# Kernel optimization log

Measured on AMD Instinct MI355X. Metric: run time of the kernel, lower is better.

Reference implementation:

```python
import math
import jax, jax.numpy as jnp
import numpy as np

G = 96       # grid side; N = G*G tokens, one token per grid cell
D = 512      # d_model
R = 2        # radius (Chebyshev)
LN_EPS = 1e-5

# 24 neighbor offsets in the (2R+1)^2 window, excluding (0,0) (self is excluded in the torch code)
_OFF = np.array([(dx, dy) for dx in range(-R, R + 1) for dy in range(-R, R + 1) if not (dx == 0 and dy == 0)], dtype=np.int32)


def _layer_norm(x, g, b):
    m = jnp.mean(x, axis=-1, keepdims=True)
    v = jnp.mean(jnp.square(x - m), axis=-1, keepdims=True)
    return (x - m) * jax.lax.rsqrt(v + LN_EPS) * g + b


def setup_inputs() -> dict:
    key = jax.random.key(0)
    ks = jax.random.split(key, 12)
    N = G * G
    x = jax.random.normal(ks[0], (N, D), jnp.float32)
    gx, gy = jnp.meshgrid(jnp.arange(G), jnp.arange(G), indexing='ij')
    grid = jnp.stack([gx.ravel(), gy.ravel()], axis=-1).astype(jnp.int32)  # [N,2], one token per cell

    def lin(k, din, dout):
        return jax.random.normal(k, (din, dout), jnp.float32) * (1.0 / math.sqrt(din))

    return {
        'x': x, 'grid': grid,
        'Wq': lin(ks[1], D, D), 'bq': jnp.zeros((D,), jnp.float32),
        'Wk': lin(ks[2], D, D), 'bk': jnp.zeros((D,), jnp.float32),
        'Wv': lin(ks[3], D, D), 'bv': jnp.zeros((D,), jnp.float32),
        'Wo': lin(ks[4], D, D), 'bo': jnp.zeros((D,), jnp.float32),
        'g1': jnp.ones((D,), jnp.float32), 'b1': jnp.zeros((D,), jnp.float32),
        'g2': jnp.ones((D,), jnp.float32), 'b2': jnp.zeros((D,), jnp.float32),
        'W1': lin(ks[5], D, 4 * D), 'bf1': jnp.zeros((4 * D,), jnp.float32),
        'W2': lin(ks[6], 4 * D, D), 'bf2': jnp.zeros((D,), jnp.float32),
    }


def reference(x, grid, Wq, bq, Wk, bk, Wv, bv, Wo, bo, g1, b1, g2, b2, W1, bf1, W2, bf2):
    # dropout is identity (eval mode)
    h = _layer_norm(x, g1, b1)
    q = h @ Wq + bq
    k = h @ Wk + bk
    v = h @ Wv + bv

    off = jnp.asarray(_OFF)                      # [K=24, 2]
    nx = grid[:, 0:1] + off[None, :, 0]          # [N, K]
    ny = grid[:, 1:2] + off[None, :, 1]
    valid = (nx >= 0) & (nx < G) & (ny >= 0) & (ny < G)
    idx = jnp.where(valid, nx * G + ny, 0)       # row-major cell -> token index

    k_nbr = k[idx]                               # [N, K, D]
    v_nbr = v[idx]                               # [N, K, D]
    scores = jnp.einsum('nd,nkd->nk', q, k_nbr) / math.sqrt(D)
    neg = jnp.finfo(scores.dtype).min
    scores = jnp.where(valid, scores, neg)
    attn = jax.nn.softmax(scores, axis=-1)       # every token has >=8 valid neighbors for G>R
    out = jnp.einsum('nk,nkd->nd', attn, v_nbr)  # [N, D]

    x = x + out @ Wo + bo
    h2 = _layer_norm(x, g2, b2)
    ffn = jax.nn.gelu(h2 @ W1 + bf1, approximate=False) @ W2 + bf2
    return x + ffn
```

## Files before the change

### kernel.cpp

```cpp
#include <hip/hip_runtime.h>

typedef unsigned short u16;
typedef unsigned int u32;
typedef __bf16 bf16x8 __attribute__((ext_vector_type(8)));
typedef float f32x4 __attribute__((ext_vector_type(4)));

#define GRID_G 96
#define DMODEL 512
#define NTOK (GRID_G * GRID_G)

__device__ __forceinline__ u16 f2bf(float f) {
  return __builtin_bit_cast(u16, (__bf16)f);
}
__device__ __forceinline__ void unpack8(uint4 u, float* f) {
  f[0] = __builtin_bit_cast(float, u.x << 16);
  f[1] = __builtin_bit_cast(float, u.x & 0xffff0000u);
  f[2] = __builtin_bit_cast(float, u.y << 16);
  f[3] = __builtin_bit_cast(float, u.y & 0xffff0000u);
  f[4] = __builtin_bit_cast(float, u.z << 16);
  f[5] = __builtin_bit_cast(float, u.z & 0xffff0000u);
  f[6] = __builtin_bit_cast(float, u.w << 16);
  f[7] = __builtin_bit_cast(float, u.w & 0xffff0000u);
}
__device__ __forceinline__ float gelu_fast(float x) {
  float y = 0.7978845608f * (x + 0.044715f * x * x * x);
  float a = fabsf(y);
  float e = __expf(-2.0f * a);
  float th = (1.0f - e) / (1.0f + e);
  th = __builtin_copysignf(th, y);
  return 0.5f * x * (1.0f + th);
}

__device__ __forceinline__ void tr_tile(const float* __restrict__ src,
                                        u16* __restrict__ dst, int R, int C,
                                        int bx, int by, float (*tile)[33]) {
  int tx = threadIdx.x & 31, ty = threadIdx.x >> 5;
#pragma unroll
  for (int i = 0; i < 4; ++i) {
    int r = ty + i * 8;
    tile[r][tx] = src[(size_t)(by * 32 + r) * C + (bx * 32 + tx)];
  }
  __syncthreads();
#pragma unroll
  for (int i = 0; i < 4; ++i) {
    int c = ty + i * 8;
    dst[(size_t)(bx * 32 + c) * R + (by * 32 + tx)] = f2bf(tile[tx][c]);
  }
}

__global__ __launch_bounds__(256) void k_prep(
    const float* __restrict__ Wq, const float* __restrict__ Wk,
    const float* __restrict__ Wv, const float* __restrict__ Wo,
    const float* __restrict__ W1, const float* __restrict__ W2,
    const float* __restrict__ bq, const float* __restrict__ bk,
    const float* __restrict__ bv, const float* __restrict__ x,
    const float* __restrict__ g1, const float* __restrict__ b1,
    u16* __restrict__ WQT, u16* __restrict__ WKT, u16* __restrict__ WVT,
    u16* __restrict__ WOT, u16* __restrict__ W1T, u16* __restrict__ W2T,
    float* __restrict__ BCAT, u16* __restrict__ H) {
  __shared__ float tile[32][33];
  const int b = blockIdx.x;
  if (b < 1024) {
    int z = b >> 8, sub = b & 255;
    const float* s = z == 0 ? Wq : z == 1 ? Wk : z == 2 ? Wv : Wo;
    u16* d = z == 0 ? WQT : z == 1 ? WKT : z == 2 ? WVT : WOT;
    tr_tile(s, d, 512, 512, sub & 15, sub >> 4, tile);
  } else if (b < 2048) {
    int idx = b - 1024;
    tr_tile(W1, W1T, 512, 2048, idx & 63, idx >> 6, tile);
  } else if (b < 3072) {
    int idx = b - 2048;
    tr_tile(W2, W2T, 2048, 512, idx & 15, idx >> 4, tile);
  } else if (b < 3078) {
    int i = (b - 3072) * 256 + threadIdx.x;
    if (i < 512) BCAT[i] = bq[i];
    else if (i < 1024) BCAT[i] = bk[i - 512];
    else if (i < 1536) BCAT[i] = bv[i - 1024];
  } else {
    int tid = threadIdx.x, wid = tid >> 6, lane = tid & 63;
    int row = (b - 3078) * 4 + wid;
    const float* xr = x + (size_t)row * DMODEL;
    float4 v0 = *(const float4*)(xr + lane * 4);
    float4 v1 = *(const float4*)(xr + 256 + lane * 4);
    float s = v0.x + v0.y + v0.z + v0.w + v1.x + v1.y + v1.z + v1.w;
    float sq = v0.x * v0.x + v0.y * v0.y + v0.z * v0.z + v0.w * v0.w +
               v1.x * v1.x + v1.y * v1.y + v1.z * v1.z + v1.w * v1.w;
#pragma unroll
    for (int m = 1; m < 64; m <<= 1) {
      s += __shfl_xor(s, m);
      sq += __shfl_xor(sq, m);
    }
    float mean = s * (1.0f / DMODEL);
    float rstd = rsqrtf(sq * (1.0f / DMODEL) - mean * mean + 1e-5f);
    float4 ga = *(const float4*)(g1 + lane * 4);
    float4 gb = *(const float4*)(g1 + 256 + lane * 4);
    float4 ba = *(const float4*)(b1 + lane * 4);
    float4 bb = *(const float4*)(b1 + 256 + lane * 4);
    ushort4 o0, o1;
    o0.x = f2bf((v0.x - mean) * rstd * ga.x + ba.x);
    o0.y = f2bf((v0.y - mean) * rstd * ga.y + ba.y);
    o0.z = f2bf((v0.z - mean) * rstd * ga.z + ba.z);
    o0.w = f2bf((v0.w - mean) * rstd * ga.w + ba.w);
    o1.x = f2bf((v1.x - mean) * rstd * gb.x + bb.x);
    o1.y = f2bf((v1.y - mean) * rstd * gb.y + bb.y);
    o1.z = f2bf((v1.z - mean) * rstd * gb.z + bb.z);
    o1.w = f2bf((v1.w - mean) * rstd * gb.w + bb.w);
    u16* op = H + (size_t)row * DMODEL;
    *(ushort4*)(op + lane * 4) = o0;
    *(ushort4*)(op + 256 + lane * 4) = o1;
  }
}

__global__ __launch_bounds__(256) void k_layernorm_bf16(
    const float* __restrict__ x, const float* __restrict__ g,
    const float* __restrict__ b, u16* __restrict__ out) {
  int tid = threadIdx.x, wid = tid >> 6, lane = tid & 63;
  int row = blockIdx.x * 4 + wid;
  const float* xr = x + (size_t)row * DMODEL;
  float4 v0 = *(const float4*)(xr + lane * 4);
  float4 v1 = *(const float4*)(xr + 256 + lane * 4);
  float s = v0.x + v0.y + v0.z + v0.w + v1.x + v1.y + v1.z + v1.w;
  float sq = v0.x * v0.x + v0.y * v0.y + v0.z * v0.z + v0.w * v0.w +
             v1.x * v1.x + v1.y * v1.y + v1.z * v1.z + v1.w * v1.w;
#pragma unroll
  for (int m = 1; m < 64; m <<= 1) {
    s += __shfl_xor(s, m);
    sq += __shfl_xor(sq, m);
  }
  float mean = s * (1.0f / DMODEL);
  float rstd = rsqrtf(sq * (1.0f / DMODEL) - mean * mean + 1e-5f);
  float4 ga = *(const float4*)(g + lane * 4);
  float4 gb = *(const float4*)(g + 256 + lane * 4);
  float4 ba = *(const float4*)(b + lane * 4);
  float4 bb = *(const float4*)(b + 256 + lane * 4);
  ushort4 o0, o1;
  o0.x = f2bf((v0.x - mean) * rstd * ga.x + ba.x);
  o0.y = f2bf((v0.y - mean) * rstd * ga.y + ba.y);
  o0.z = f2bf((v0.z - mean) * rstd * ga.z + ba.z);
  o0.w = f2bf((v0.w - mean) * rstd * ga.w + ba.w);
  o1.x = f2bf((v1.x - mean) * rstd * gb.x + bb.x);
  o1.y = f2bf((v1.y - mean) * rstd * gb.y + bb.y);
  o1.z = f2bf((v1.z - mean) * rstd * gb.z + bb.z);
  o1.w = f2bf((v1.w - mean) * rstd * gb.w + bb.w);
  u16* op = out + (size_t)row * DMODEL;
  *(ushort4*)(op + lane * 4) = o0;
  *(ushort4*)(op + 256 + lane * 4) = o1;
}

__global__ __launch_bounds__(256) void k_attn(
    const u16* __restrict__ q, const u16* __restrict__ kk,
    const u16* __restrict__ vv, const int* __restrict__ gpos,
    u16* __restrict__ out) {
  int tid = threadIdx.x, wid = tid >> 6, lane = tid & 63;
  int n = blockIdx.x * 4 + wid;
  int px = gpos[2 * n], py = gpos[2 * n + 1];
  float qf[8];
  unpack8(*(const uint4*)(q + (size_t)n * DMODEL + lane * 8), qf);
  float sc[24];
  int nid[24];
  bool ok[24];
#pragma unroll
  for (int j = 0; j < 24; ++j) {
    int jj = j < 12 ? j : j + 1;
    int dx = jj / 5 - 2, dy = jj % 5 - 2;
    int nx = px + dx, ny = py + dy;
    bool val = (nx >= 0) && (nx < GRID_G) && (ny >= 0) && (ny < GRID_G);
    int id = val ? nx * GRID_G + ny : 0;
    ok[j] = val;
    nid[j] = id;
    float kf[8];
    unpack8(*(const uint4*)(kk + (size_t)id * DMODEL + lane * 8), kf);
    float p = 0.f;
#pragma unroll
    for (int e = 0; e < 8; ++e) p += qf[e] * kf[e];
#pragma unroll
    for (int m = 1; m < 64; m <<= 1) p += __shfl_xor(p, m);
    sc[j] = p * 0.04419417382415922f;
  }
  float mx = -3.0e38f;
#pragma unroll
  for (int j = 0; j < 24; ++j)
    if (ok[j]) mx = fmaxf(mx, sc[j]);
  float wsum = 0.f, w[24];
#pragma unroll
  for (int j = 0; j < 24; ++j) {
    w[j] = ok[j] ? expf(sc[j] - mx) : 0.f;
    wsum += w[j];
  }
  float inv = 1.0f / wsum;
  float acc[8] = {0, 0, 0, 0, 0, 0, 0, 0};
#pragma unroll
  for (int j = 0; j < 24; ++j) {
    float vf[8];
    unpack8(*(const uint4*)(vv + (size_t)nid[j] * DMODEL + lane * 8), vf);
    float wj = w[j];
#pragma unroll
    for (int e = 0; e < 8; ++e) acc[e] += wj * vf[e];
  }
  uint4 o;
  o.x = (u32)f2bf(acc[0] * inv) | ((u32)f2bf(acc[1] * inv) << 16);
  o.y = (u32)f2bf(acc[2] * inv) | ((u32)f2bf(acc[3] * inv) << 16);
  o.z = (u32)f2bf(acc[4] * inv) | ((u32)f2bf(acc[5] * inv) << 16);
  o.w = (u32)f2bf(acc[6] * inv) | ((u32)f2bf(acc[7] * inv) << 16);
  *(uint4*)(out + (size_t)n * DMODEL + lane * 8) = o;
}

#define BARR { __builtin_amdgcn_s_barrier(); __builtin_amdgcn_sched_barrier(0); }
#define WAIT8 asm volatile("s_waitcnt vmcnt(8)" ::: "memory");
#define WAIT0 asm volatile("s_waitcnt vmcnt(0)" ::: "memory");
#define LGKM0 asm volatile("s_waitcnt lgkmcnt(0)" ::: "memory");

template <int EPI>
__global__ __launch_bounds__(256, 2) void k_gemm(
    const u16* __restrict__ A, const u16* __restrict__ Bt,
    const float* __restrict__ bias, const float* __restrict__ res,
    float* __restrict__ outF, u16* __restrict__ outB,
    int M, int N, int K, int tiles_n) {
  __shared__ u16 lds[32768];
  const int t = threadIdx.x, wid = t >> 6, lane = t & 63;
  const int nwg = gridDim.x, bid = blockIdx.x;
  const int l = ((bid & 7) * (nwg >> 3)) + (bid >> 3);
  const int bM = (l / tiles_n) * 128, bN = (l % tiles_n) * 128;
  const int wr = wid >> 1, wc = wid & 1, lr = lane & 15, lg = lane >> 4;

  const int rs = lane >> 3;
  const int cl = (lane & 7) ^ rs;
  const u16* gA[4];
  const u16* gB[4];
  int dstL[4];
#pragma unroll
  for (int j = 0; j < 4; ++j) {
    int r = wid * 32 + j * 8 + rs;
    gA[j] = A + (size_t)(bM + r) * K + cl * 8;
    gB[j] = Bt + (size_t)(bN + r) * K + cl * 8;
    dstL[j] = wid * 2048 + j * 512;
  }

#define STAGE1(BUF, KOFF)                                                             \
  {                                                                                   \
    _Pragma("unroll") for (int j = 0; j < 4; ++j) {                                   \
      __builtin_amdgcn_global_load_lds(                                               \
          (const __attribute__((address_space(1))) void*)(gA[j] + (KOFF)),            \
          (__attribute__((address_space(3))) void*)(lds + (BUF)*16384 + dstL[j]),     \
          16, 0, 0);                                                                  \
      __builtin_amdgcn_global_load_lds(                                               \
          (const __attribute__((address_space(1))) void*)(gB[j] + (KOFF)),            \
          (__attribute__((address_space(3))) void*)(lds + (BUF)*16384 + 8192 + dstL[j]), \
          16, 0, 0);                                                                  \
    }                                                                                 \
  }

  const int offA0 = (wr * 64 + lr) * 64 + ((0 + lg) ^ (lr & 7)) * 8;
  const int offA1 = (wr * 64 + lr) * 64 + ((4 + lg) ^ (lr & 7)) * 8;
  const int offB0 = (wc * 64 + lr) * 64 + ((0 + lg) ^ (lr & 7)) * 8;
  const int offB1 = (wc * 64 + lr) * 64 + ((4 + lg) ^ (lr & 7)) * 8;

  f32x4 acc[4][4];
#pragma unroll
  for (int i = 0; i < 4; ++i)
#pragma unroll
    for (int j = 0; j < 4; ++j) acc[i][j] = (f32x4){0.f, 0.f, 0.f, 0.f};

#define COMPUTE1(BUF)                                                                 \
  {                                                                                   \
    _Pragma("unroll") for (int ks = 0; ks < 2; ++ks) {                                \
      const int oa = (BUF)*16384 + (ks ? offA1 : offA0);                              \
      const int ob = (BUF)*16384 + 8192 + (ks ? offB1 : offB0);                       \
      bf16x8 af[4], bfr[4];                                                           \
      _Pragma("unroll") for (int mt = 0; mt < 4; ++mt)                                \
          af[mt] = __builtin_bit_cast(bf16x8, *(const uint4*)(lds + oa + mt * 1024)); \
      _Pragma("unroll") for (int nt = 0; nt < 4; ++nt)                                \
          bfr[nt] = __builtin_bit_cast(bf16x8, *(const uint4*)(lds + ob + nt * 1024));\
      _Pragma("unroll") for (int mt = 0; mt < 4; ++mt)                                \
          _Pragma("unroll") for (int nt = 0; nt < 4; ++nt)                            \
              acc[mt][nt] = __builtin_amdgcn_mfma_f32_16x16x32_bf16(                  \
                  af[mt], bfr[nt], acc[mt][nt], 0, 0, 0);                             \
    }                                                                                 \
  }

  const int nk = K >> 6;
  STAGE1(0, 0);
  int koff = 64;
  for (int tt = 0; tt < nk; tt += 2) {
    if (tt + 1 < nk) { STAGE1(1, koff); WAIT8 } else { WAIT0 }
    BARR;
    COMPUTE1(0);
    BARR;
    if (tt + 2 < nk) { STAGE1(0, koff + 64); WAIT8 } else { WAIT0 }
    BARR;
    COMPUTE1(1);
    BARR;
    koff += 128;
  }
#undef STAGE1
#undef COMPUTE1

#pragma unroll
  for (int mt = 0; mt < 4; ++mt) {
#pragma unroll
    for (int nt = 0; nt < 4; ++nt) {
      int col = bN + wc * 64 + nt * 16 + lr;
      float bc = bias[col];
      int row0 = bM + wr * 64 + mt * 16 + lg * 4;
#pragma unroll
      for (int r = 0; r < 4; ++r) {
        float val = acc[mt][nt][r] + bc;
        size_t off = (size_t)(row0 + r) * N + col;
        if constexpr (EPI == 1) {
          outF[off] = res[off] + val;
        } else {
          outB[off] = f2bf(val);
        }
      }
    }
  }
}

template <int EPI>
__global__ __launch_bounds__(256, 4) void k_gemm_hi(
    const u16* __restrict__ A, const u16* __restrict__ Bt,
    const float* __restrict__ bias, u16* __restrict__ outB,
    int M, int N, int K, int tiles_n) {
  __shared__ u16 lds[16384];
  const int t = threadIdx.x, wid = t >> 6, lane = t & 63;
  const int nwg = gridDim.x, bid = blockIdx.x;
  const int l = ((bid & 7) * (nwg >> 3)) + (bid >> 3);
  const int bM = (l / tiles_n) * 128, bN = (l % tiles_n) * 128;
  const int wr = wid >> 1, wc = wid & 1, lr = lane & 15, lg = lane >> 4;

  const int rs = lane >> 3;
  const int cl = (lane & 7) ^ rs;
  const u16* gA[4];
  const u16* gB[4];
  int dstL[4];
#pragma unroll
  for (int j = 0; j < 4; ++j) {
    int r = wid * 32 + j * 8 + rs;
    gA[j] = A + (size_t)(bM + r) * K + cl * 8;
    gB[j] = Bt + (size_t)(bN + r) * K + cl * 8;
    dstL[j] = wid * 2048 + j * 512;
  }

  const int offA0 = (wr * 64 + lr) * 64 + ((0 + lg) ^ (lr & 7)) * 8;
  const int offA1 = (wr * 64 + lr) * 64 + ((4 + lg) ^ (lr & 7)) * 8;
  const int offB0 = 8192 + (wc * 64 + lr) * 64 + ((0 + lg) ^ (lr & 7)) * 8;
  const int offB1 = 8192 + (wc * 64 + lr) * 64 + ((4 + lg) ^ (lr & 7)) * 8;

  f32x4 acc[4][4];
#pragma unroll
  for (int i = 0; i < 4; ++i)
#pragma unroll
    for (int j = 0; j < 4; ++j) acc[i][j] = (f32x4){0.f, 0.f, 0.f, 0.f};

  const int nk = K >> 6;
  for (int tt = 0; tt < nk; ++tt) {
    const int koff = tt << 6;
#pragma unroll
    for (int j = 0; j < 4; ++j) {
      __builtin_amdgcn_global_load_lds(
          (const __attribute__((address_space(1))) void*)(gA[j] + koff),
          (__attribute__((address_space(3))) void*)(lds + dstL[j]), 16, 0, 0);
      __builtin_amdgcn_global_load_lds(
          (const __attribute__((address_space(1))) void*)(gB[j] + koff),
          (__attribute__((address_space(3))) void*)(lds + 8192 + dstL[j]), 16, 0, 0);
    }
    WAIT0;
    BARR;
#pragma unroll
    for (int ks = 0; ks < 2; ++ks) {
      const int oa = ks ? offA1 : offA0;
      const int ob = ks ? offB1 : offB0;
      bf16x8 af[4], bfr[4];
#pragma unroll
      for (int mt = 0; mt < 4; ++mt)
        af[mt] = __builtin_bit_cast(bf16x8, *(const uint4*)(lds + oa + mt * 1024));
#pragma unroll
      for (int nt = 0; nt < 4; ++nt)
        bfr[nt] = __builtin_bit_cast(bf16x8, *(const uint4*)(lds + ob + nt * 1024));
#pragma unroll
      for (int mt = 0; mt < 4; ++mt)
#pragma unroll
        for (int nt = 0; nt < 4; ++nt)
          acc[mt][nt] = __builtin_amdgcn_mfma_f32_16x16x32_bf16(af[mt], bfr[nt], acc[mt][nt], 0, 0, 0);
    }
    LGKM0;
    BARR;
  }

#pragma unroll
  for (int mt = 0; mt < 4; ++mt) {
#pragma unroll
    for (int nt = 0; nt < 4; ++nt) {
      int col = bN + wc * 64 + nt * 16 + lr;
      float bc = bias[col];
      int row0 = bM + wr * 64 + mt * 16 + lg * 4;
#pragma unroll
      for (int r = 0; r < 4; ++r) {
        float val = acc[mt][nt][r] + bc;
        if constexpr (EPI == 2) {
          outB[(size_t)(row0 + r) * N + col] = f2bf(gelu_fast(val));
        } else {
          int seg = col >> 9;
          size_t off = (size_t)seg * ((size_t)NTOK * DMODEL) +
                       (size_t)(row0 + r) * DMODEL + (col & 511);
          outB[off] = f2bf(val);
        }
      }
    }
  }
}

extern "C" void kernel_launch(void* const* d_in, const int* in_sizes, int n_in,
                              void* d_out, int out_size, void* d_ws, size_t ws_size,
                              hipStream_t stream) {
  const float* x = (const float*)d_in[0];
  const int* gpos = (const int*)d_in[1];
  const float* Wq = (const float*)d_in[2];
  const float* bq = (const float*)d_in[3];
  const float* Wk = (const float*)d_in[4];
  const float* bk = (const float*)d_in[5];
  const float* Wv = (const float*)d_in[6];
  const float* bv = (const float*)d_in[7];
  const float* Wo = (const float*)d_in[8];
  const float* bo = (const float*)d_in[9];
  const float* g1 = (const float*)d_in[10];
  const float* b1 = (const float*)d_in[11];
  const float* g2 = (const float*)d_in[12];
  const float* b2 = (const float*)d_in[13];
  const float* W1 = (const float*)d_in[14];
  const float* bf1 = (const float*)d_in[15];
  const float* W2 = (const float*)d_in[16];
  const float* bf2 = (const float*)d_in[17];
  float* out = (float*)d_out;
  char* ws = (char*)d_ws;

  constexpr size_t SZ_W512 = (size_t)512 * 512 * 2;
  constexpr size_t SZ_W2048 = (size_t)512 * 2048 * 2;
  constexpr size_t SZ_ACT = (size_t)NTOK * 512 * 2;

  u16* WQT = (u16*)(ws + 0);
  u16* WKT = (u16*)(ws + SZ_W512);
  u16* WVT = (u16*)(ws + 2 * SZ_W512);
  u16* WOT = (u16*)(ws + 3 * SZ_W512);
  u16* W1T = (u16*)(ws + 4 * SZ_W512);
  u16* W2T = (u16*)(ws + 4 * SZ_W512 + SZ_W2048);
  float* BCAT = (float*)(ws + 4 * SZ_W512 + 2 * SZ_W2048);
  char* actbase = ws + 4 * SZ_W512 + 2 * SZ_W2048 + 6144;
  u16* H = (u16*)(actbase);
  u16* Q = (u16*)(actbase + SZ_ACT);
  u16* KB = (u16*)(actbase + 2 * SZ_ACT);
  u16* VB = (u16*)(actbase + 3 * SZ_ACT);
  u16* H2 = (u16*)(actbase + 4 * SZ_ACT);
  u16* U = (u16*)(actbase);

  k_prep<<<5382, 256, 0, stream>>>(Wq, Wk, Wv, Wo, W1, W2, bq, bk, bv, x, g1, b1,
                                   WQT, WKT, WVT, WOT, W1T, W2T, BCAT, H);

  k_gemm_hi<3><<<864, 256, 0, stream>>>(H, WQT, BCAT, Q, NTOK, 1536, 512, 12);

  k_attn<<<NTOK / 4, 256, 0, stream>>>(Q, KB, VB, gpos, H);

  k_gemm<1><<<288, 256, 0, stream>>>(H, WOT, bo, x, out, nullptr, NTOK, 512, 512, 4);

  k_layernorm_bf16<<<NTOK / 4, 256, 0, stream>>>(out, g2, b2, H2);

  k_gemm_hi<2><<<1152, 256, 0, stream>>>(H2, W1T, bf1, U, NTOK, 2048, 512, 16);

  k_gemm<1><<<288, 256, 0, stream>>>(U, W2T, bf2, out, out, nullptr, NTOK, 512, 2048, 4);
}
```

Baseline: 158.9 us.

## Use 256x128 GEMM tiles with 8 waves sharing B tile, fast softmax intrinsics

The QKV and FFN1 GEMMs move from 128x128 tiles with 4 waves to 256x128 tiles with 8 waves. The B tile is loaded into LDS once and shared across twice as many rows, which cuts global and L2 traffic for the weights and halves the grid size. K is now a template constant so the loop bound is known at compile time. The attention softmax also switches to the fast __expf and a hardware reciprocal, trading a little accuracy for fewer instructions; the larger LDS footprint and 512-thread blocks may lower occupancy.

After: 156.1 us. No clear change (-1.7%).

```diff
diff --git a/kernel.cpp b/kernel.cpp
--- a/kernel.cpp
+++ b/kernel.cpp
@@ -184,10 +184,10 @@
   float wsum = 0.f, w[24];
 #pragma unroll
   for (int j = 0; j < 24; ++j) {
-    w[j] = ok[j] ? expf(sc[j] - mx) : 0.f;
+    w[j] = ok[j] ? __expf(sc[j] - mx) : 0.f;
     wsum += w[j];
   }
-  float inv = 1.0f / wsum;
+  float inv = __builtin_amdgcn_rcpf(wsum);
   float acc[8] = {0, 0, 0, 0, 0, 0, 0, 0};
 #pragma unroll
   for (int j = 0; j < 24; ++j) {
@@ -316,35 +316,28 @@
   }
 }
 
-template <int EPI>
-__global__ __launch_bounds__(256, 4) void k_gemm_hi(
+template <int EPI, int KDIM>
+__global__ __launch_bounds__(512, 4) void k_gemm_hi2(
     const u16* __restrict__ A, const u16* __restrict__ Bt,
     const float* __restrict__ bias, u16* __restrict__ outB,
-    int M, int N, int K, int tiles_n) {
-  __shared__ u16 lds[16384];
-  const int t = threadIdx.x, wid = t >> 6, lane = t & 63;
+    int N, int tiles_n) {
+  __shared__ u16 lds[24576];
+  const int t = threadIdx.x, w = t >> 6, lane = t & 63;
   const int nwg = gridDim.x, bid = blockIdx.x;
   const int l = ((bid & 7) * (nwg >> 3)) + (bid >> 3);
-  const int bM = (l / tiles_n) * 128, bN = (l % tiles_n) * 128;
-  const int wr = wid >> 1, wc = wid & 1, lr = lane & 15, lg = lane >> 4;
+  const int bM = (l / tiles_n) * 256, bN = (l % tiles_n) * 128;
+  const int wr = w >> 1, wc = w & 1, lr = lane & 15, lg = lane >> 4;
 
   const int rs = lane >> 3;
   const int cl = (lane & 7) ^ rs;
-  const u16* gA[4];
-  const u16* gB[4];
-  int dstL[4];
-#pragma unroll
-  for (int j = 0; j < 4; ++j) {
-    int r = wid * 32 + j * 8 + rs;
-    gA[j] = A + (size_t)(bM + r) * K + cl * 8;
-    gB[j] = Bt + (size_t)(bN + r) * K + cl * 8;
-    dstL[j] = wid * 2048 + j * 512;
-  }
+  const u16* pA = A + (size_t)(bM + w * 8 + rs) * KDIM + cl * 8;
+  const u16* pB = Bt + (size_t)(bN + w * 8 + rs) * KDIM + cl * 8;
+  const int dbase = w * 512;
 
   const int offA0 = (wr * 64 + lr) * 64 + ((0 + lg) ^ (lr & 7)) * 8;
   const int offA1 = (wr * 64 + lr) * 64 + ((4 + lg) ^ (lr & 7)) * 8;
-  const int offB0 = 8192 + (wc * 64 + lr) * 64 + ((0 + lg) ^ (lr & 7)) * 8;
-  const int offB1 = 8192 + (wc * 64 + lr) * 64 + ((4 + lg) ^ (lr & 7)) * 8;
+  const int offB0 = 16384 + (wc * 64 + lr) * 64 + ((0 + lg) ^ (lr & 7)) * 8;
+  const int offB1 = 16384 + (wc * 64 + lr) * 64 + ((4 + lg) ^ (lr & 7)) * 8;
 
   f32x4 acc[4][4];
 #pragma unroll
@@ -352,18 +345,19 @@
 #pragma unroll
     for (int j = 0; j < 4; ++j) acc[i][j] = (f32x4){0.f, 0.f, 0.f, 0.f};
 
-  const int nk = K >> 6;
+  constexpr int nk = KDIM >> 6;
   for (int tt = 0; tt < nk; ++tt) {
     const int koff = tt << 6;
 #pragma unroll
-    for (int j = 0; j < 4; ++j) {
+    for (int j = 0; j < 4; ++j)
       __builtin_amdgcn_global_load_lds(
-          (const __attribute__((address_space(1))) void*)(gA[j] + koff),
-          (__attribute__((address_space(3))) void*)(lds + dstL[j]), 16, 0, 0);
+          (const __attribute__((address_space(1))) void*)(pA + (size_t)j * 64 * KDIM + koff),
+          (__attribute__((address_space(3))) void*)(lds + j * 4096 + dbase), 16, 0, 0);
+#pragma unroll
+    for (int j = 0; j < 2; ++j)
       __builtin_amdgcn_global_load_lds(
-          (const __attribute__((address_space(1))) void*)(gB[j] + koff),
-          (__attribute__((address_space(3))) void*)(lds + 8192 + dstL[j]), 16, 0, 0);
-    }
+          (const __attribute__((address_space(1))) void*)(pB + (size_t)j * 64 * KDIM + koff),
+          (__attribute__((address_space(3))) void*)(lds + 16384 + j * 4096 + dbase), 16, 0, 0);
     WAIT0;
     BARR;
 #pragma unroll
@@ -456,7 +450,7 @@
   k_prep<<<5382, 256, 0, stream>>>(Wq, Wk, Wv, Wo, W1, W2, bq, bk, bv, x, g1, b1,
                                    WQT, WKT, WVT, WOT, W1T, W2T, BCAT, H);
 
-  k_gemm_hi<3><<<864, 256, 0, stream>>>(H, WQT, BCAT, Q, NTOK, 1536, 512, 12);
+  k_gemm_hi2<3, 512><<<432, 512, 0, stream>>>(H, WQT, BCAT, Q, 1536, 12);
 
   k_attn<<<NTOK / 4, 256, 0, stream>>>(Q, KB, VB, gpos, H);
 
@@ -464,7 +458,7 @@
 
   k_layernorm_bf16<<<NTOK / 4, 256, 0, stream>>>(out, g2, b2, H2);
 
-  k_gemm_hi<2><<<1152, 256, 0, stream>>>(H2, W1T, bf1, U, NTOK, 2048, 512, 16);
+  k_gemm_hi2<2, 512><<<576, 512, 0, stream>>>(H2, W1T, bf1, U, 2048, 16);
 
   k_gemm<1><<<288, 256, 0, stream>>>(U, W2T, bf2, out, out, nullptr, NTOK, 512, 2048, 4);
 }
```
